# Performance work log

Hardware: AMD Instinct MI355X
Metric: run time of the kernel (lower is better)

The kernel has to match this reference:

```python
import jax, jax.numpy as jnp
import numpy as np

N_NODES = 50000
N_EDGES = 800000
VOCAB = 15000
IN_FEATS = 128
HIDDEN = 32
HEADS = 4
N_GRAPHS = 64
NEG_SLOPE = 0.2


def setup_inputs() -> dict:
    key = jax.random.key(0)
    ks = jax.random.split(key, 16)
    word_ids = jax.random.randint(ks[0], (N_NODES,), 0, VOCAB)
    edge_src = jax.random.randint(ks[1], (N_EDGES,), 0, N_NODES)
    edge_dst = jax.random.randint(ks[2], (N_EDGES,), 0, N_NODES)
    node_graph_id = jnp.sort(jax.random.randint(ks[3], (N_NODES,), 0, N_GRAPHS))
    y_data = jax.random.uniform(ks[4], (N_GRAPHS,))
    word_embeds = jax.random.normal(ks[5], (VOCAB, IN_FEATS)) * 0.02
    W0 = jax.random.normal(ks[6], (IN_FEATS, HEADS * HIDDEN)) * (1.0 / np.sqrt(IN_FEATS))
    al0 = jax.random.normal(ks[7], (HEADS, HIDDEN)) * 0.1
    ar0 = jax.random.normal(ks[8], (HEADS, HIDDEN)) * 0.1
    W1 = jax.random.normal(ks[9], (HEADS * HIDDEN, HEADS * HIDDEN)) * (1.0 / np.sqrt(HEADS * HIDDEN))
    al1 = jax.random.normal(ks[10], (HEADS, HIDDEN)) * 0.1
    ar1 = jax.random.normal(ks[11], (HEADS, HIDDEN)) * 0.1
    out_w = jax.random.normal(ks[12], (HEADS * HIDDEN, 1)) * (1.0 / np.sqrt(HEADS * HIDDEN))
    out_b = jnp.zeros((1,))
    return {"word_ids": word_ids, "edge_src": edge_src, "edge_dst": edge_dst,
            "node_graph_id": node_graph_id, "y_data": y_data,
            "word_embeds": word_embeds, "W0": W0, "al0": al0, "ar0": ar0,
            "W1": W1, "al1": al1, "ar1": ar1, "out_w": out_w, "out_b": out_b}


def gat_layer(h, src, dst, W, al, ar):
    # h: [N, Fin] -> feat: [N, H, D]
    feat = (h @ W).reshape(N_NODES, HEADS, HIDDEN)
    el = (feat * al[None]).sum(-1)  # [N, H]
    er = (feat * ar[None]).sum(-1)  # [N, H]
    e = jax.nn.leaky_relu(el[src] + er[dst], NEG_SLOPE)  # [E, H]
    # segment softmax over incoming edges of each dst node
    m = jax.ops.segment_max(e, dst, num_segments=N_NODES)
    m = jnp.where(jnp.isfinite(m), m, 0.0)
    ex = jnp.exp(e - m[dst])
    denom = jax.ops.segment_sum(ex, dst, num_segments=N_NODES)
    alpha = ex / (denom[dst] + 1e-10)  # [E, H]
    msg = feat[src] * alpha[:, :, None]  # [E, H, D]
    out = jax.ops.segment_sum(msg, dst, num_segments=N_NODES)  # [N, H, D]
    return jax.nn.elu(out).reshape(N_NODES, HEADS * HIDDEN)


def reference(word_ids, edge_src, edge_dst, node_graph_id, y_data,
              word_embeds, W0, al0, ar0, W1, al1, ar1, out_w, out_b):
    h = word_embeds[word_ids]  # [N, IN_FEATS]
    h = gat_layer(h, edge_src, edge_dst, W0, al0, ar0)
    h = gat_layer(h, edge_src, edge_dst, W1, al1, ar1)
    # per-graph max pooling over nodes
    pooled = jax.ops.segment_max(h, node_graph_id, num_segments=N_GRAPHS)
    pooled = jnp.where(jnp.isfinite(pooled), pooled, 0.0)  # guard empty graphs
    logits = (pooled @ out_w + out_b).reshape(-1)  # [G]
    # BCE with logits (stable)
    loss = jnp.mean(jnp.maximum(logits, 0.0) - logits * y_data
                    + jnp.log1p(jnp.exp(-jnp.abs(logits))))
    y_pred = jax.nn.sigmoid(logits)[:, None]
    return (loss, y_pred)
```

## Files before the change

### kernel.cpp

```cpp
#include <hip/hip_runtime.h>
#include <math.h>

#define N_NODES 50000
#define N_EDGES 800000
#define HEADS 4
#define N_GRAPHS 64
#define NEG_SLOPE 0.2f
#define LOG2E 1.4426950408889634f
#define SCAN_NB 196
#define POOL_CHUNK 200
#define POOL_NB 250
#define FEAT_NB 782
#define EDGE_Q 200000
#define EDGE_NB 782

typedef __attribute__((ext_vector_type(8))) short bf16x8;
typedef __attribute__((ext_vector_type(4))) float f32x4;

__device__ __forceinline__ unsigned fkey(float f) {
    unsigned u = __float_as_uint(f);
    return (u & 0x80000000u) ? ~u : (u | 0x80000000u);
}
__device__ __forceinline__ float kval(unsigned k) {
    unsigned u = (k & 0x80000000u) ? (k & 0x7FFFFFFFu) : ~k;
    return __uint_as_float(u);
}

__device__ __forceinline__ unsigned short f2bf(float f) {
    unsigned u = __float_as_uint(f);
    u += 0x7FFFu + ((u >> 16) & 1u);
    return (unsigned short)(u >> 16);
}
__device__ __forceinline__ unsigned pack_bf2(float a, float b) {
    return (unsigned)f2bf(a) | ((unsigned)f2bf(b) << 16);
}


__global__ void hist_kernel(const int* __restrict__ dst, int* __restrict__ deg,
                            int* __restrict__ rank) {
    int i = blockIdx.x * 256 + threadIdx.x;
    if (i >= EDGE_Q) return;
    int e0 = i, e1 = i + EDGE_Q, e2 = i + 2 * EDGE_Q, e3 = i + 3 * EDGE_Q;
    int d0 = dst[e0], d1 = dst[e1], d2 = dst[e2], d3 = dst[e3];
    int r0 = atomicAdd(&deg[d0], 1);
    int r1 = atomicAdd(&deg[d1], 1);
    int r2 = atomicAdd(&deg[d2], 1);
    int r3 = atomicAdd(&deg[d3], 1);
    rank[e0] = r0; rank[e1] = r1; rank[e2] = r2; rank[e3] = r3;
}

__global__ void partial_kernel(const int* __restrict__ deg, int* __restrict__ partial) {
    int t = threadIdx.x, b = blockIdx.x;
    int i = b * 256 + t;
    int v = (i < N_NODES) ? deg[i] : 0;
    #pragma unroll
    for (int off = 1; off < 64; off <<= 1) v += __shfl_xor(v, off, 64);
    __shared__ int wsum[4];
    if ((t & 63) == 0) wsum[t >> 6] = v;
    __syncthreads();
    if (t == 0) partial[b] = wsum[0] + wsum[1] + wsum[2] + wsum[3];
}

__global__ void csr_offsets_kernel(const int* __restrict__ deg, const int* __restrict__ partial,
                                   int* __restrict__ row_start) {
    __shared__ int sb[SCAN_NB];
    __shared__ int wsumA[4];
    __shared__ int wsumB[4];
    int t = threadIdx.x, b = blockIdx.x;
    int lane = t & 63, w = t >> 6;
    {
        int v = (t < SCAN_NB) ? partial[t] : 0;
        int incl = v;
        #pragma unroll
        for (int off = 1; off < 64; off <<= 1) {
            int u = __shfl_up(incl, off, 64);
            if (lane >= off) incl += u;
        }
        if (lane == 63) wsumA[w] = incl;
        __syncthreads();
        int woff = 0;
        #pragma unroll
        for (int k = 0; k < 4; ++k) if (k < w) woff += wsumA[k];
        if (t < SCAN_NB) sb[t] = woff + incl - v;
        __syncthreads();
    }
    int i = b * 256 + t;
    int v = (i < N_NODES) ? deg[i] : 0;
    int incl = v;
    #pragma unroll
    for (int off = 1; off < 64; off <<= 1) {
        int u = __shfl_up(incl, off, 64);
        if (lane >= off) incl += u;
    }
    if (lane == 63) wsumB[w] = incl;
    __syncthreads();
    int woff = sb[b];
    #pragma unroll
    for (int k = 0; k < 4; ++k) if (k < w) woff += wsumB[k];
    int excl = woff + incl - v;
    if (i < N_NODES) row_start[i] = excl;
    else if (i == N_NODES) row_start[i] = excl;
}

__global__ void scatter_kernel(const int* __restrict__ src, const int* __restrict__ dst,
                               const int* __restrict__ rank, const int* __restrict__ row_start,
                               int* __restrict__ csr_src) {
    int i = blockIdx.x * 256 + threadIdx.x;
    if (i >= EDGE_Q) return;
    int e0 = i, e1 = i + EDGE_Q, e2 = i + 2 * EDGE_Q, e3 = i + 3 * EDGE_Q;
    int d0 = dst[e0], d1 = dst[e1], d2 = dst[e2], d3 = dst[e3];
    int k0 = rank[e0], k1 = rank[e1], k2 = rank[e2], k3 = rank[e3];
    int s0 = src[e0], s1 = src[e1], s2 = src[e2], s3 = src[e3];
    csr_src[row_start[d0] + k0] = s0;
    csr_src[row_start[d1] + k1] = s1;
    csr_src[row_start[d2] + k2] = s2;
    csr_src[row_start[d3] + k3] = s3;
}


__global__ void wfrag_kernel(const float* __restrict__ W, unsigned* __restrict__ wf) {
    int slot = blockIdx.x * 256 + threadIdx.x;
    int f = slot >> 6, l = slot & 63;
    int n = l & 15, q = l >> 4;
    int ct = f >> 2, kq = f & 3;
    int col = 16 * ct + n;
    int k0 = 32 * kq + 8 * q;
    uint4 o;
    o.x = pack_bf2(W[(k0 + 0) * 128 + col], W[(k0 + 1) * 128 + col]);
    o.y = pack_bf2(W[(k0 + 2) * 128 + col], W[(k0 + 3) * 128 + col]);
    o.z = pack_bf2(W[(k0 + 4) * 128 + col], W[(k0 + 5) * 128 + col]);
    o.w = pack_bf2(W[(k0 + 6) * 128 + col], W[(k0 + 7) * 128 + col]);
    ((uint4*)wf)[slot] = o;
}

__global__ __launch_bounds__(256)
void feat_kernel(const float* __restrict__ h, const int* __restrict__ wid,
                 const unsigned* __restrict__ wf,
                 const float* __restrict__ al, const float* __restrict__ ar,
                 unsigned* __restrict__ featb, float* __restrict__ el,
                 float* __restrict__ er) {
    __shared__ unsigned hl[64 * 68];
    int t = threadIdx.x;
    int n0 = blockIdx.x * 64;
    const float4* h4 = (const float4*)h;
    #pragma unroll
    for (int r = 0; r < 8; ++r) {
        int i = t + 256 * r;
        int n = i >> 5, q4 = i & 31;
        float4 v = {0.f, 0.f, 0.f, 0.f};
        int gn = n0 + n;
        if (gn < N_NODES) {
            int row = wid ? wid[gn] : gn;
            v = h4[(size_t)row * 32 + q4];
        }
        hl[n * 68 + q4 * 2]     = pack_bf2(v.x, v.y);
        hl[n * 68 + q4 * 2 + 1] = pack_bf2(v.z, v.w);
    }
    __syncthreads();
    int w = t >> 6, lane = t & 63;
    int col = lane & 15, quad = lane >> 4;
    int nbase = n0 + 16 * w;
    bf16x8 afr[4];
    #pragma unroll
    for (int kq = 0; kq < 4; ++kq)
        afr[kq] = *(const bf16x8*)&hl[(16 * w + col) * 68 + 16 * kq + 4 * quad];
    f32x4 acc[8];
    #pragma unroll
    for (int ct = 0; ct < 8; ++ct) acc[ct] = (f32x4){0.f, 0.f, 0.f, 0.f};
    const uint4* wf4 = (const uint4*)wf;
    #pragma unroll
    for (int ct = 0; ct < 8; ++ct) {
        #pragma unroll
        for (int kq = 0; kq < 4; ++kq) {
            uint4 braw = wf4[(ct * 4 + kq) * 64 + lane];
            bf16x8 bfr = *(const bf16x8*)&braw;
            acc[ct] = __builtin_amdgcn_mfma_f32_16x16x32_bf16(afr[kq], bfr, acc[ct], 0, 0, 0);
        }
    }
    #pragma unroll
    for (int ct = 0; ct < 8; ++ct) {
        #pragma unroll
        for (int reg = 0; reg < 4; ++reg) {
            float v = acc[ct][reg];
            float pv = __shfl_xor(v, 1, 64);
            int node = nbase + quad * 4 + reg;
            if (!(col & 1) && node < N_NODES)
                featb[(size_t)node * 64 + ct * 8 + (col >> 1)] = pack_bf2(v, pv);
        }
    }
    float alv[8], arv[8];
    #pragma unroll
    for (int ct = 0; ct < 8; ++ct) {
        alv[ct] = al[ct * 16 + col];
        arv[ct] = ar[ct * 16 + col];
    }
    #pragma unroll
    for (int reg = 0; reg < 4; ++reg) {
        int node = nbase + quad * 4 + reg;
        #pragma unroll
        for (int hd = 0; hd < 4; ++hd) {
            float pl = acc[2 * hd][reg] * alv[2 * hd] + acc[2 * hd + 1][reg] * alv[2 * hd + 1];
            float pr = acc[2 * hd][reg] * arv[2 * hd] + acc[2 * hd + 1][reg] * arv[2 * hd + 1];
            #pragma unroll
            for (int off = 1; off < 16; off <<= 1) {
                pl += __shfl_xor(pl, off, 64);
                pr += __shfl_xor(pr, off, 64);
            }
            if (col == hd && node < N_NODES) {
                el[node * 4 + hd] = pl * LOG2E;
                er[node * 4 + hd] = pr * LOG2E;
            }
        }
    }
}

__global__ void gat_aggregate(const int* __restrict__ row_start, const int* __restrict__ csr_src,
                              const unsigned* __restrict__ featb, const float* __restrict__ el,
                              const float* __restrict__ er, float* __restrict__ hout) {
    int lane = threadIdx.x & 63;
    int d = blockIdx.x * 4 + (threadIdx.x >> 6);
    int beg = row_start[d], end = row_start[d + 1];
    int eg = lane >> 4;
    int li = lane & 15;
    int hc = li >> 2;
    float er_h = er[d * 4 + hc];
    float a0 = 0.f, a1 = 0.f, a2 = 0.f, a3 = 0.f;
    float a4 = 0.f, a5 = 0.f, a6 = 0.f, a7 = 0.f;
    float dsum = 0.f;
    int b8 = beg + ((end - beg) & ~7);
    for (int base = beg; base < b8; base += 8) {
        int ea = base + eg, eb = base + 4 + eg;
        int sa = csr_src[ea];
        int sb = csr_src[eb];
        float la = el[sa * 4 + hc];
        float lb = el[sb * 4 + hc];
        uint4 pa = *(const uint4*)(featb + (size_t)sa * 64 + li * 4);
        uint4 pb = *(const uint4*)(featb + (size_t)sb * 64 + li * 4);
        float va = la + er_h; va = fmaxf(va, NEG_SLOPE * va);
        float vb = lb + er_h; vb = fmaxf(vb, NEG_SLOPE * vb);
        float xa = exp2f(va), xb = exp2f(vb);
        dsum += xa + xb;
        a0 += __uint_as_float(pa.x << 16) * xa;
        a1 += __uint_as_float(pa.x & 0xFFFF0000u) * xa;
        a2 += __uint_as_float(pa.y << 16) * xa;
        a3 += __uint_as_float(pa.y & 0xFFFF0000u) * xa;
        a4 += __uint_as_float(pa.z << 16) * xa;
        a5 += __uint_as_float(pa.z & 0xFFFF0000u) * xa;
        a6 += __uint_as_float(pa.w << 16) * xa;
        a7 += __uint_as_float(pa.w & 0xFFFF0000u) * xa;
        a0 += __uint_as_float(pb.x << 16) * xb;
        a1 += __uint_as_float(pb.x & 0xFFFF0000u) * xb;
        a2 += __uint_as_float(pb.y << 16) * xb;
        a3 += __uint_as_float(pb.y & 0xFFFF0000u) * xb;
        a4 += __uint_as_float(pb.z << 16) * xb;
        a5 += __uint_as_float(pb.z & 0xFFFF0000u) * xb;
        a6 += __uint_as_float(pb.w << 16) * xb;
        a7 += __uint_as_float(pb.w & 0xFFFF0000u) * xb;
    }
    for (int ee = b8 + eg; ee < end; ee += 4) {
        int s = csr_src[ee];
        float lv = el[s * 4 + hc];
        uint4 pv = *(const uint4*)(featb + (size_t)s * 64 + li * 4);
        float v = lv + er_h; v = fmaxf(v, NEG_SLOPE * v);
        float x = exp2f(v);
        dsum += x;
        a0 += __uint_as_float(pv.x << 16) * x;
        a1 += __uint_as_float(pv.x & 0xFFFF0000u) * x;
        a2 += __uint_as_float(pv.y << 16) * x;
        a3 += __uint_as_float(pv.y & 0xFFFF0000u) * x;
        a4 += __uint_as_float(pv.z << 16) * x;
        a5 += __uint_as_float(pv.z & 0xFFFF0000u) * x;
        a6 += __uint_as_float(pv.w << 16) * x;
        a7 += __uint_as_float(pv.w & 0xFFFF0000u) * x;
    }
    #pragma unroll
    for (int off = 16; off < 64; off <<= 1) {
        a0 += __shfl_xor(a0, off, 64);
        a1 += __shfl_xor(a1, off, 64);
        a2 += __shfl_xor(a2, off, 64);
        a3 += __shfl_xor(a3, off, 64);
        a4 += __shfl_xor(a4, off, 64);
        a5 += __shfl_xor(a5, off, 64);
        a6 += __shfl_xor(a6, off, 64);
        a7 += __shfl_xor(a7, off, 64);
        dsum += __shfl_xor(dsum, off, 64);
    }
    if (eg == 0) {
        float inv = 1.f / (dsum + 1e-10f);
        float o0 = a0 * inv, o1 = a1 * inv, o2 = a2 * inv, o3 = a3 * inv;
        float o4 = a4 * inv, o5 = a5 * inv, o6 = a6 * inv, o7 = a7 * inv;
        o0 = o0 > 0.f ? o0 : expm1f(o0);
        o1 = o1 > 0.f ? o1 : expm1f(o1);
        o2 = o2 > 0.f ? o2 : expm1f(o2);
        o3 = o3 > 0.f ? o3 : expm1f(o3);
        o4 = o4 > 0.f ? o4 : expm1f(o4);
        o5 = o5 > 0.f ? o5 : expm1f(o5);
        o6 = o6 > 0.f ? o6 : expm1f(o6);
        o7 = o7 > 0.f ? o7 : expm1f(o7);
        float4* op = (float4*)(hout + (size_t)d * 128);
        float4 w0 = {o0, o1, o2, o3};
        float4 w1 = {o4, o5, o6, o7};
        op[li * 2] = w0;
        op[li * 2 + 1] = w1;
    }
}


__global__ void pool_kernel(const int* __restrict__ gid, const float* __restrict__ h,
                            unsigned* __restrict__ pkeys) {
    int t = threadIdx.x;
    int c = t & 127;
    int par = t >> 7;
    int n0 = blockIdx.x * POOL_CHUNK;
    float m = 0.f;
    int cur_g = -1;
    for (int n = n0 + par; n < n0 + POOL_CHUNK; n += 2) {
        int g = gid[n];
        if (g != cur_g) {
            if (cur_g >= 0) atomicMax(&pkeys[cur_g * 128 + c], fkey(m));
            cur_g = g;
            m = -3.0e38f;
        }
        m = fmaxf(m, h[(size_t)n * 128 + c]);
    }
    if (cur_g >= 0) atomicMax(&pkeys[cur_g * 128 + c], fkey(m));
}

__global__ void logits_kernel(const unsigned* __restrict__ pkeys, const float* __restrict__ w,
                              const float* __restrict__ bptr, float* __restrict__ logits) {
    int g = blockIdx.x, t = threadIdx.x;
    float sum = 0.f;
    for (int c = t; c < 128; c += 64) {
        unsigned k = pkeys[g * 128 + c];
        float v = (k == 0u) ? 0.f : kval(k);
        sum += v * w[c];
    }
    #pragma unroll
    for (int off = 32; off; off >>= 1) sum += __shfl_down(sum, off, 64);
    if (t == 0) logits[g] = sum + bptr[0];
}

__global__ void final_kernel(const float* __restrict__ logits, const float* __restrict__ y,
                             float* __restrict__ out) {
    int t = threadIdx.x;
    float l = logits[t];
    float term = fmaxf(l, 0.f) - l * y[t] + log1pf(expf(-fabsf(l)));
    float s = term;
    #pragma unroll
    for (int off = 32; off; off >>= 1) s += __shfl_down(s, off, 64);
    out[1 + t] = 1.f / (1.f + expf(-l));
    if (t == 0) out[0] = s * (1.f / 64.f);
}

extern "C" void kernel_launch(void* const* d_in, const int* in_sizes, int n_in,
                              void* d_out, int out_size, void* d_ws, size_t ws_size,
                              hipStream_t stream) {
    const int* word_ids  = (const int*)d_in[0];
    const int* esrc      = (const int*)d_in[1];
    const int* edst      = (const int*)d_in[2];
    const int* gid       = (const int*)d_in[3];
    const float* y_data  = (const float*)d_in[4];
    const float* emb     = (const float*)d_in[5];
    const float* W0      = (const float*)d_in[6];
    const float* al0     = (const float*)d_in[7];
    const float* ar0     = (const float*)d_in[8];
    const float* W1      = (const float*)d_in[9];
    const float* al1     = (const float*)d_in[10];
    const float* ar1     = (const float*)d_in[11];
    const float* out_w   = (const float*)d_in[12];
    const float* out_b   = (const float*)d_in[13];
    float* out = (float*)d_out;

    float* ws = (float*)d_ws;
    unsigned* featb  = (unsigned*)ws;
    float*    hbuf   = ws + 3200000;
    float*    el     = ws + 9600000;
    float*    er     = ws + 9800000;
    int*      row_st = (int*)(ws + 10000000);
    int*      deg    = (int*)(ws + 10051000);
    int*      rank   = (int*)(ws + 10101000);
    int*      csrsrc = (int*)(ws + 10901000);
    int*      partial= (int*)(ws + 11701000);
    unsigned* pkeys  = (unsigned*)(ws + 11701400);
    float*    logits = ws + 11709592;
    unsigned* wfbuf  = (unsigned*)(ws + 11709704);

    hipMemsetAsync(deg, 0, (size_t)N_NODES * 4, stream);
    hist_kernel<<<EDGE_NB, 256, 0, stream>>>(edst, deg, rank);
    partial_kernel<<<SCAN_NB, 256, 0, stream>>>(deg, partial);
    csr_offsets_kernel<<<SCAN_NB, 256, 0, stream>>>(deg, partial, row_st);
    scatter_kernel<<<EDGE_NB, 256, 0, stream>>>(esrc, edst, rank, row_st, csrsrc);

    wfrag_kernel<<<8, 256, 0, stream>>>(W0, wfbuf);
    feat_kernel<<<FEAT_NB, 256, 0, stream>>>(emb, word_ids, wfbuf, al0, ar0, featb, el, er);
    gat_aggregate<<<12500, 256, 0, stream>>>(row_st, csrsrc, featb, el, er, hbuf);
    wfrag_kernel<<<8, 256, 0, stream>>>(W1, wfbuf);
    feat_kernel<<<FEAT_NB, 256, 0, stream>>>(hbuf, nullptr, wfbuf, al1, ar1, featb, el, er);
    gat_aggregate<<<12500, 256, 0, stream>>>(row_st, csrsrc, featb, el, er, hbuf);

    hipMemsetAsync(pkeys, 0, (size_t)N_GRAPHS * 128 * 4, stream);
    pool_kernel<<<POOL_NB, 256, 0, stream>>>(gid, hbuf, pkeys);
    logits_kernel<<<N_GRAPHS, 64, 0, stream>>>(pkeys, out_w, out_b, logits);
    final_kernel<<<1, 64, 0, stream>>>(logits, y_data, out);
}
```

Measured before the change: 302.5 us.

## Fuse prep kernels, overlap scatter with layer-0 features, bf16 intermediate activations

```diff
diff --git a/kernel.cpp b/kernel.cpp
--- a/kernel.cpp
+++ b/kernel.cpp
@@ -102,10 +102,12 @@
     else if (i == N_NODES) row_start[i] = excl;
 }
 
-__global__ void scatter_kernel(const int* __restrict__ src, const int* __restrict__ dst,
-                               const int* __restrict__ rank, const int* __restrict__ row_start,
-                               int* __restrict__ csr_src) {
-    int i = blockIdx.x * 256 + threadIdx.x;
+__device__ __forceinline__ void scatter_body(int bid, const int* __restrict__ src,
+                                             const int* __restrict__ dst,
+                                             const int* __restrict__ rank,
+                                             const int* __restrict__ row_start,
+                                             int* __restrict__ csr_src) {
+    int i = bid * 256 + threadIdx.x;
     if (i >= EDGE_Q) return;
     int e0 = i, e1 = i + EDGE_Q, e2 = i + 2 * EDGE_Q, e3 = i + 3 * EDGE_Q;
     int d0 = dst[e0], d1 = dst[e1], d2 = dst[e2], d3 = dst[e3];
@@ -118,8 +120,8 @@
 }
 
 
-__global__ void wfrag_kernel(const float* __restrict__ W, unsigned* __restrict__ wf) {
-    int slot = blockIdx.x * 256 + threadIdx.x;
+__device__ __forceinline__ void wfrag_body(const float* __restrict__ W,
+                                           unsigned* __restrict__ wf, int slot) {
     int f = slot >> 6, l = slot & 63;
     int n = l & 15, q = l >> 4;
     int ct = f >> 2, kq = f & 3;
@@ -133,28 +135,60 @@
     ((uint4*)wf)[slot] = o;
 }
 
-__global__ __launch_bounds__(256)
-void feat_kernel(const float* __restrict__ h, const int* __restrict__ wid,
-                 const unsigned* __restrict__ wf,
-                 const float* __restrict__ al, const float* __restrict__ ar,
-                 unsigned* __restrict__ featb, float* __restrict__ el,
-                 float* __restrict__ er) {
+__global__ void prep_kernel(const float* __restrict__ W0, const float* __restrict__ W1,
+                            unsigned* __restrict__ wf0, unsigned* __restrict__ wf1,
+                            int* __restrict__ deg, unsigned* __restrict__ pkeys) {
+    int b = blockIdx.x, t = threadIdx.x;
+    if (b < 8) {
+        wfrag_body(W0, wf0, b * 256 + t);
+    } else if (b < 16) {
+        wfrag_body(W1, wf1, (b - 8) * 256 + t);
+    } else if (b < 16 + SCAN_NB) {
+        int i = (b - 16) * 256 + t;
+        if (i < N_NODES) deg[i] = 0;
+    } else {
+        int i = (b - 16 - SCAN_NB) * 256 + t;
+        if (i < N_GRAPHS * 128) pkeys[i] = 0;
+    }
+}
+
+template<int IN_BF16>
+__device__ __forceinline__ void feat_body(int bid, const void* __restrict__ hin,
+                                          const int* __restrict__ wid,
+                                          const unsigned* __restrict__ wf,
+                                          const float* __restrict__ al,
+                                          const float* __restrict__ ar,
+                                          unsigned* __restrict__ featb,
+                                          float* __restrict__ el, float* __restrict__ er) {
     __shared__ unsigned hl[64 * 68];
     int t = threadIdx.x;
-    int n0 = blockIdx.x * 64;
-    const float4* h4 = (const float4*)h;
-    #pragma unroll
-    for (int r = 0; r < 8; ++r) {
-        int i = t + 256 * r;
-        int n = i >> 5, q4 = i & 31;
-        float4 v = {0.f, 0.f, 0.f, 0.f};
-        int gn = n0 + n;
-        if (gn < N_NODES) {
-            int row = wid ? wid[gn] : gn;
-            v = h4[(size_t)row * 32 + q4];
-        }
-        hl[n * 68 + q4 * 2]     = pack_bf2(v.x, v.y);
-        hl[n * 68 + q4 * 2 + 1] = pack_bf2(v.z, v.w);
+    int n0 = bid * 64;
+    if (IN_BF16) {
+        const uint4* hb4 = (const uint4*)hin;
+        #pragma unroll
+        for (int r = 0; r < 4; ++r) {
+            int i = t + 256 * r;
+            int n = i >> 4, q = i & 15;
+            uint4 v = {0u, 0u, 0u, 0u};
+            int gn = n0 + n;
+            if (gn < N_NODES) v = hb4[(size_t)gn * 16 + q];
+            *(uint4*)&hl[n * 68 + q * 4] = v;
+        }
+    } else {
+        const float4* h4 = (const float4*)hin;
+        #pragma unroll
+        for (int r = 0; r < 8; ++r) {
+            int i = t + 256 * r;
+            int n = i >> 5, q4 = i & 31;
+            float4 v = {0.f, 0.f, 0.f, 0.f};
+            int gn = n0 + n;
+            if (gn < N_NODES) {
+                int row = wid ? wid[gn] : gn;
+                v = h4[(size_t)row * 32 + q4];
+            }
+            hl[n * 68 + q4 * 2]     = pack_bf2(v.x, v.y);
+            hl[n * 68 + q4 * 2 + 1] = pack_bf2(v.z, v.w);
+        }
     }
     __syncthreads();
     int w = t >> 6, lane = t & 63;
@@ -214,9 +248,37 @@
     }
 }
 
-__global__ void gat_aggregate(const int* __restrict__ row_start, const int* __restrict__ csr_src,
-                              const unsigned* __restrict__ featb, const float* __restrict__ el,
-                              const float* __restrict__ er, float* __restrict__ hout) {
+template<int IN_BF16>
+__global__ __launch_bounds__(256)
+void feat_kernel_t(const void* __restrict__ hin, const int* __restrict__ wid,
+                   const unsigned* __restrict__ wf,
+                   const float* __restrict__ al, const float* __restrict__ ar,
+                   unsigned* __restrict__ featb, float* __restrict__ el,
+                   float* __restrict__ er) {
+    feat_body<IN_BF16>(blockIdx.x, hin, wid, wf, al, ar, featb, el, er);
+}
+
+__global__ __launch_bounds__(256)
+void scatter_feat0_kernel(const int* __restrict__ src, const int* __restrict__ dst,
+                          const int* __restrict__ rank, const int* __restrict__ row_start,
+                          int* __restrict__ csr_src,
+                          const float* __restrict__ emb, const int* __restrict__ wid,
+                          const unsigned* __restrict__ wf0,
+                          const float* __restrict__ al0, const float* __restrict__ ar0,
+                          unsigned* __restrict__ featb, float* __restrict__ el,
+                          float* __restrict__ er) {
+    if (blockIdx.x < EDGE_NB) {
+        scatter_body(blockIdx.x, src, dst, rank, row_start, csr_src);
+    } else {
+        feat_body<0>(blockIdx.x - EDGE_NB, emb, wid, wf0, al0, ar0, featb, el, er);
+    }
+}
+
+template<int OUT_BF16>
+__global__ void gat_aggregate_t(const int* __restrict__ row_start, const int* __restrict__ csr_src,
+                                const unsigned* __restrict__ featb, const float* __restrict__ el,
+                                const float* __restrict__ er, float* __restrict__ houtf,
+                                unsigned* __restrict__ houtb) {
     int lane = threadIdx.x & 63;
     int d = blockIdx.x * 4 + (threadIdx.x >> 6);
     int beg = row_start[d], end = row_start[d + 1];
@@ -297,11 +359,20 @@
         o5 = o5 > 0.f ? o5 : expm1f(o5);
         o6 = o6 > 0.f ? o6 : expm1f(o6);
         o7 = o7 > 0.f ? o7 : expm1f(o7);
-        float4* op = (float4*)(hout + (size_t)d * 128);
-        float4 w0 = {o0, o1, o2, o3};
-        float4 w1 = {o4, o5, o6, o7};
-        op[li * 2] = w0;
-        op[li * 2 + 1] = w1;
+        if (OUT_BF16) {
+            uint4 wv;
+            wv.x = pack_bf2(o0, o1);
+            wv.y = pack_bf2(o2, o3);
+            wv.z = pack_bf2(o4, o5);
+            wv.w = pack_bf2(o6, o7);
+            ((uint4*)(houtb + (size_t)d * 64))[li] = wv;
+        } else {
+            float4* op = (float4*)(houtf + (size_t)d * 128);
+            float4 w0 = {o0, o1, o2, o3};
+            float4 w1 = {o4, o5, o6, o7};
+            op[li * 2] = w0;
+            op[li * 2 + 1] = w1;
+        }
     }
 }
 
@@ -326,30 +397,38 @@
     if (cur_g >= 0) atomicMax(&pkeys[cur_g * 128 + c], fkey(m));
 }
 
-__global__ void logits_kernel(const unsigned* __restrict__ pkeys, const float* __restrict__ w,
-                              const float* __restrict__ bptr, float* __restrict__ logits) {
-    int g = blockIdx.x, t = threadIdx.x;
-    float sum = 0.f;
-    for (int c = t; c < 128; c += 64) {
-        unsigned k = pkeys[g * 128 + c];
-        float v = (k == 0u) ? 0.f : kval(k);
-        sum += v * w[c];
-    }
-    #pragma unroll
-    for (int off = 32; off; off >>= 1) sum += __shfl_down(sum, off, 64);
-    if (t == 0) logits[g] = sum + bptr[0];
-}
-
-__global__ void final_kernel(const float* __restrict__ logits, const float* __restrict__ y,
-                             float* __restrict__ out) {
+__global__ void logits_final_kernel(const unsigned* __restrict__ pkeys,
+                                    const float* __restrict__ w, const float* __restrict__ bptr,
+                                    const float* __restrict__ y, float* __restrict__ out) {
+    __shared__ float slog[N_GRAPHS];
     int t = threadIdx.x;
-    float l = logits[t];
-    float term = fmaxf(l, 0.f) - l * y[t] + log1pf(expf(-fabsf(l)));
-    float s = term;
-    #pragma unroll
-    for (int off = 32; off; off >>= 1) s += __shfl_down(s, off, 64);
-    out[1 + t] = 1.f / (1.f + expf(-l));
-    if (t == 0) out[0] = s * (1.f / 64.f);
+    int wv = t >> 6, lane = t & 63;
+    float b = bptr[0];
+    #pragma unroll
+    for (int k = 0; k < 16; ++k) {
+        int g = wv * 16 + k;
+        float sum = 0.f;
+        #pragma unroll
+        for (int c0 = 0; c0 < 128; c0 += 64) {
+            int c = c0 + lane;
+            unsigned kk = pkeys[g * 128 + c];
+            float v = (kk == 0u) ? 0.f : kval(kk);
+            sum += v * w[c];
+        }
+        #pragma unroll
+        for (int off = 32; off; off >>= 1) sum += __shfl_down(sum, off, 64);
+        if (lane == 0) slog[g] = sum + b;
+    }
+    __syncthreads();
+    if (t < N_GRAPHS) {
+        float l = slog[t];
+        float term = fmaxf(l, 0.f) - l * y[t] + log1pf(expf(-fabsf(l)));
+        float s = term;
+        #pragma unroll
+        for (int off = 32; off; off >>= 1) s += __shfl_down(s, off, 64);
+        out[1 + t] = 1.f / (1.f + expf(-l));
+        if (t == 0) out[0] = s * (1.f / 64.f);
+    }
 }
 
 extern "C" void kernel_launch(void* const* d_in, const int* in_sizes, int n_in,
@@ -373,33 +452,31 @@
 
     float* ws = (float*)d_ws;
     unsigned* featb  = (unsigned*)ws;
-    float*    hbuf   = ws + 3200000;
-    float*    el     = ws + 9600000;
-    float*    er     = ws + 9800000;
-    int*      row_st = (int*)(ws + 10000000);
-    int*      deg    = (int*)(ws + 10051000);
-    int*      rank   = (int*)(ws + 10101000);
-    int*      csrsrc = (int*)(ws + 10901000);
-    int*      partial= (int*)(ws + 11701000);
-    unsigned* pkeys  = (unsigned*)(ws + 11701400);
-    float*    logits = ws + 11709592;
-    unsigned* wfbuf  = (unsigned*)(ws + 11709704);
-
-    hipMemsetAsync(deg, 0, (size_t)N_NODES * 4, stream);
+    unsigned* hb     = (unsigned*)(ws + 3200000);
+    float*    hout   = ws + 6400000;
+    float*    el     = ws + 12800000;
+    float*    er     = ws + 13000000;
+    int*      row_st = (int*)(ws + 13200000);
+    int*      deg    = (int*)(ws + 13250004);
+    int*      rank   = (int*)(ws + 13300004);
+    int*      csrsrc = (int*)(ws + 14100004);
+    int*      partial= (int*)(ws + 14900004);
+    unsigned* pkeys  = (unsigned*)(ws + 14900204);
+    unsigned* wf0    = (unsigned*)(ws + 14908396);
+    unsigned* wf1    = (unsigned*)(ws + 14916588);
+
+    prep_kernel<<<16 + SCAN_NB + 32, 256, 0, stream>>>(W0, W1, wf0, wf1, deg, pkeys);
     hist_kernel<<<EDGE_NB, 256, 0, stream>>>(edst, deg, rank);
     partial_kernel<<<SCAN_NB, 256, 0, stream>>>(deg, partial);
     csr_offsets_kernel<<<SCAN_NB, 256, 0, stream>>>(deg, partial, row_st);
-    scatter_kernel<<<EDGE_NB, 256, 0, stream>>>(esrc, edst, rank, row_st, csrsrc);
-
-    wfrag_kernel<<<8, 256, 0, stream>>>(W0, wfbuf);
-    feat_kernel<<<FEAT_NB, 256, 0, stream>>>(emb, word_ids, wfbuf, al0, ar0, featb, el, er);
-    gat_aggregate<<<12500, 256, 0, stream>>>(row_st, csrsrc, featb, el, er, hbuf);
-    wfrag_kernel<<<8, 256, 0, stream>>>(W1, wfbuf);
-    feat_kernel<<<FEAT_NB, 256, 0, stream>>>(hbuf, nullptr, wfbuf, al1, ar1, featb, el, er);
-    gat_aggregate<<<12500, 256, 0, stream>>>(row_st, csrsrc, featb, el, er, hbuf);
-
-    hipMemsetAsync(pkeys, 0, (size_t)N_GRAPHS * 128 * 4, stream);
-    pool_kernel<<<POOL_NB, 256, 0, stream>>>(gid, hbuf, pkeys);
-    logits_kernel<<<N_GRAPHS, 64, 0, stream>>>(pkeys, out_w, out_b, logits);
-    final_kernel<<<1, 64, 0, stream>>>(logits, y_data, out);
-}
+
+    scatter_feat0_kernel<<<EDGE_NB + FEAT_NB, 256, 0, stream>>>(
+        esrc, edst, rank, row_st, csrsrc, emb, word_ids, wf0, al0, ar0, featb, el, er);
+
+    gat_aggregate_t<1><<<12500, 256, 0, stream>>>(row_st, csrsrc, featb, el, er, nullptr, hb);
+    feat_kernel_t<1><<<FEAT_NB, 256, 0, stream>>>(hb, nullptr, wf1, al1, ar1, featb, el, er);
+    gat_aggregate_t<0><<<12500, 256, 0, stream>>>(row_st, csrsrc, featb, el, er, hout, nullptr);
+
+    pool_kernel<<<POOL_NB, 256, 0, stream>>>(gid, hout, pkeys);
+    logits_final_kernel<<<1, 256, 0, stream>>>(pkeys, out_w, out_b, y_data, out);
+}
```

Result: no change. 297.9 us (-1.5%).
